# Kernel optimization log

Hardware: AMD Instinct MI355X
Metric: run time of the kernel (lower is better)

Reference implementation:

```python
import jax, jax.numpy as jnp
import numpy as np

H = 1024          # hidden_size
I = 2048          # intermediate_size
E = 8             # num_experts
K = 2             # num_experts_per_token
B, S = 4, 4096


def setup_inputs() -> dict:
    key = jax.random.key(0)
    ks = jax.random.split(key, 5)
    scale = 0.02
    return {
        "hidden_states": jax.random.normal(ks[0], (B, S, H), dtype=jnp.float32),
        "gate_w": jax.random.normal(ks[1], (H, E), dtype=jnp.float32) * scale,      # router gate (Linear, no bias), stored [in,out]
        "gate_proj_w": jax.random.normal(ks[2], (E, H, I), dtype=jnp.float32) * scale,
        "up_proj_w": jax.random.normal(ks[3], (E, H, I), dtype=jnp.float32) * scale,
        "down_proj_w": jax.random.normal(ks[4], (E, I, H), dtype=jnp.float32) * scale,
    }


def reference(hidden_states, gate_w, gate_proj_w, up_proj_w, down_proj_w):
    b, s, h = hidden_states.shape
    x = hidden_states.reshape(-1, h)                      # (T, H), T = b*s
    T = x.shape[0]

    # --- Router: softmax over experts, top-k, renormalize ---
    logits = x @ gate_w                                    # (T, E)
    probs = jax.nn.softmax(logits, axis=-1)
    topk_w, topk_idx = jax.lax.top_k(probs, K)             # (T, K)
    topk_w = topk_w / jnp.sum(topk_w, axis=-1, keepdims=True)

    # Per-token combine weight for each expert (0 if not routed).
    # topk indices are distinct, so scatter-add == scatter-set here.
    combine = jnp.zeros((T, E), dtype=x.dtype).at[
        jnp.arange(T)[:, None], topk_idx
    ].add(topk_w)                                          # (T, E)

    # --- Experts: SwiGLU FFN, weighted combine ---
    out = jnp.zeros_like(x)
    for e in range(E):  # small fixed expert count
        g = jax.nn.silu(x @ gate_proj_w[e])                # (T, I)
        u = x @ up_proj_w[e]                               # (T, I)
        y = (g * u) @ down_proj_w[e]                       # (T, H)
        out = out + y * combine[:, e:e + 1]
    return out.reshape(b, s, h)
```

## Files before the change

### kernel.cpp

```cpp
#include <hip/hip_runtime.h>
#include <hip/hip_bf16.h>

#define T_TOK 16384
#define H_DIM 1024
#define I_DIM 2048
#define E_NUM 8

typedef short short8 __attribute__((ext_vector_type(8)));
typedef float f32x4 __attribute__((ext_vector_type(4)));

__device__ __forceinline__ unsigned short f2bf(float f) {
  union { float f; unsigned u; } v; v.f = f;
  unsigned r = (v.u + 0x7FFFu + ((v.u >> 16) & 1u)) >> 16;
  return (unsigned short)r;
}
__device__ __forceinline__ float bf2f(unsigned short u) {
  union { unsigned u; float f; } v; v.u = ((unsigned)u) << 16;
  return v.f;
}

__device__ __forceinline__ void gload16(const void* g, void* l) {
  __builtin_amdgcn_global_load_lds(
      (const __attribute__((address_space(1))) unsigned int*)g,
      (__attribute__((address_space(3))) unsigned int*)l, 16, 0, 0);
}

#define VMCNT4() asm volatile("s_waitcnt vmcnt(4)" ::: "memory")
#define VMCNT0() asm volatile("s_waitcnt vmcnt(0)" ::: "memory")
#define BAR() __builtin_amdgcn_s_barrier()
#define SCHEDFENCE() __builtin_amdgcn_sched_barrier(0)

__global__ __launch_bounds__(256) void convert_router_kernel(
    const float* __restrict__ x, const float* __restrict__ gw,
    unsigned short* __restrict__ xb,
    int* __restrict__ tke, float* __restrict__ pwv) {
  const int tid = threadIdx.x;
  const int lane = tid & 63;
  const int wv = tid >> 6;
  const int t = blockIdx.x * 4 + wv;
  const float* xr = x + (size_t)t * H_DIM;
  unsigned short* xbr = xb + (size_t)t * H_DIM;

  float acc[8] = {0.f, 0.f, 0.f, 0.f, 0.f, 0.f, 0.f, 0.f};
#pragma unroll
  for (int i = 0; i < 4; ++i) {
    int h0 = i * 256 + lane * 4;
    float4 v = *(const float4*)(xr + h0);
    ushort4 o;
    o.x = f2bf(v.x); o.y = f2bf(v.y); o.z = f2bf(v.z); o.w = f2bf(v.w);
    *(ushort4*)(xbr + h0) = o;
    float vv[4] = {v.x, v.y, v.z, v.w};
#pragma unroll
    for (int j = 0; j < 4; ++j) {
      const float4 g0 = *(const float4*)(gw + (size_t)(h0 + j) * 8);
      const float4 g1 = *(const float4*)(gw + (size_t)(h0 + j) * 8 + 4);
      acc[0] += vv[j] * g0.x; acc[1] += vv[j] * g0.y;
      acc[2] += vv[j] * g0.z; acc[3] += vv[j] * g0.w;
      acc[4] += vv[j] * g1.x; acc[5] += vv[j] * g1.y;
      acc[6] += vv[j] * g1.z; acc[7] += vv[j] * g1.w;
    }
  }
#pragma unroll
  for (int e = 0; e < 8; ++e) {
#pragma unroll
    for (int off = 32; off; off >>= 1) acc[e] += __shfl_xor(acc[e], off);
  }
  int e1 = 0; float l1 = acc[0];
#pragma unroll
  for (int e = 1; e < 8; ++e) if (acc[e] > l1) { l1 = acc[e]; e1 = e; }
  int first_non = (e1 == 0) ? 1 : 0;
  int e2 = first_non; float l2 = acc[first_non];
#pragma unroll
  for (int e = 0; e < 8; ++e) {
    if (e == e1 || e == first_non) continue;
    if (acc[e] > l2) { l2 = acc[e]; e2 = e; }
  }
  float r = expf(l2 - l1);
  float w1 = 1.f / (1.f + r);
  float w2 = r / (1.f + r);
  if (lane == 0) {
    pwv[2 * t] = w1;
    pwv[2 * t + 1] = w2;
    tke[t] = e1 | (e2 << 4);
  }
}

__global__ __launch_bounds__(256) void build_lists_kernel(
    const int* __restrict__ tke, int* __restrict__ list, int* __restrict__ cnt) {
  const int t = blockIdx.x * 256 + threadIdx.x;
  const int lane = threadIdx.x & 63;
  const int pk = tke[t];
  const int ee[2] = {pk & 15, (pk >> 4) & 15};
#pragma unroll
  for (int phase = 0; phase < 2; ++phase) {
    const int e = ee[phase];
    const int pid = 2 * t + phase;
#pragma unroll
    for (int ex = 0; ex < E_NUM; ++ex) {
      unsigned long long mask = __ballot(e == ex);
      if (e == ex) {
        unsigned long long below = mask & ((1ull << lane) - 1ull);
        int rank = __popcll(below);
        int leader = __ffsll((unsigned long long)mask) - 1;
        int base = 0;
        if (lane == leader) base = atomicAdd(&cnt[ex], __popcll(mask));
        base = __shfl(base, leader);
        list[ex * T_TOK + base + rank] = pid;
      }
    }
  }
}

__global__ __launch_bounds__(256) void transpose_convert(
    const float* __restrict__ src, unsigned short* __restrict__ dst, int K, int N) {
  __shared__ float t[128][65];
  const int e = blockIdx.x, kt = blockIdx.y, nt = blockIdx.z;
  const float* s = src + (size_t)e * K * N + (size_t)(kt * 128) * N + nt * 64;
  unsigned short* d = dst + (size_t)e * N * K + (size_t)(nt * 64) * K + kt * 128;
  const int tid = threadIdx.x;
  const int lr = tid & 15, row = tid >> 4;
#pragma unroll
  for (int p = 0; p < 8; ++p) {
    int k = row + p * 16;
    float4 v = *(const float4*)(s + (size_t)k * N + lr * 4);
    t[k][lr * 4 + 0] = v.x;
    t[k][lr * 4 + 1] = v.y;
    t[k][lr * 4 + 2] = v.z;
    t[k][lr * 4 + 3] = v.w;
  }
  __syncthreads();
  const int kc = tid & 15, nr = tid >> 4;
#pragma unroll
  for (int p = 0; p < 4; ++p) {
    int n = nr + p * 16;
    short8 o;
#pragma unroll
    for (int j = 0; j < 8; ++j) o[j] = (short)f2bf(t[kc * 8 + j][n]);
    *(short8*)&d[(size_t)n * K + kc * 8] = o;
  }
}

__global__ __launch_bounds__(256, 3) void gemm_gateup(
    const unsigned short* __restrict__ xb, const unsigned short* __restrict__ wgt,
    const unsigned short* __restrict__ wut, const int* __restrict__ list,
    const int* __restrict__ cnt, const float* __restrict__ pwv,
    unsigned short* __restrict__ hbuf) {
  __shared__ unsigned short As[2][128 * 32];
  __shared__ unsigned short Bg[2][64 * 32];
  __shared__ unsigned short Bu[2][64 * 32];
  __shared__ int rows_s[128];
  __shared__ float pws[128];

  const int tid = threadIdx.x;
  const int e = blockIdx.y >> 7;
  const int mt = blockIdx.y & 127;
  const int ce = cnt[e];
  if (mt * 128 >= ce) return;
  const int n0 = blockIdx.x * 64;

  if (tid < 128) {
    int idx = mt * 128 + tid;
    int pid = list[e * T_TOK + (idx < ce ? idx : 0)];
    rows_s[tid] = pid;
    pws[tid] = pwv[pid];
  }
  __syncthreads();

  const int s0 = tid, s1 = 256 + tid;
  const int q0 = (((s0 & 3) ^ ((s0 >> 3) & 3)) * 8);
  const int q1 = (((s1 & 3) ^ ((s1 >> 3) & 3)) * 8);
  const int tok0 = rows_s[s0 >> 2] >> 1, tok1 = rows_s[s1 >> 2] >> 1;

  const unsigned short* wg_base = wgt + ((size_t)e * I_DIM + n0) * H_DIM;
  const unsigned short* wu_base = wut + ((size_t)e * I_DIM + n0) * H_DIM;
  const unsigned short* a_src0 = xb + (size_t)tok0 * H_DIM + q0;
  const unsigned short* a_src1 = xb + (size_t)tok1 * H_DIM + q1;
  const unsigned short* g_src0 = wg_base + (size_t)(s0 >> 2) * H_DIM + q0;
  const unsigned short* u_src0 = wu_base + (size_t)(s0 >> 2) * H_DIM + q0;

#define STAGE_GU(b, k0)                         \
  do {                                          \
    gload16(a_src0 + (k0), &As[b][s0 * 8]);     \
    gload16(a_src1 + (k0), &As[b][s1 * 8]);     \
    gload16(g_src0 + (k0), &Bg[b][s0 * 8]);     \
    gload16(u_src0 + (k0), &Bu[b][s0 * 8]);     \
  } while (0)

  f32x4 zero = {0.f, 0.f, 0.f, 0.f};
  f32x4 accg[4][2], accu[4][2];
#pragma unroll
  for (int m = 0; m < 4; ++m)
#pragma unroll
    for (int n = 0; n < 2; ++n) { accg[m][n] = zero; accu[m][n] = zero; }

  const int lane = tid & 63;
  const int wv = tid >> 6;
  const int wr = (wv >> 1) * 64;
  const int wc = (wv & 1) * 32;
  const int lr = lane & 15;
  const int lks = (((lane >> 4) ^ ((lr >> 1) & 3)) * 8);

  STAGE_GU(0, 0);

  for (int kt = 0; kt < H_DIM / 32; ++kt) {
    const int cur = kt & 1;
    if (kt < H_DIM / 32 - 1) {
      STAGE_GU(cur ^ 1, (kt + 1) * 32);
      VMCNT4();
    } else {
      VMCNT0();
    }
    BAR();
    SCHEDFENCE();
    const unsigned short* Ab = As[cur];
    const unsigned short* Bgb = Bg[cur];
    const unsigned short* Bub = Bu[cur];
    short8 a[4], bg[2], bu[2];
#pragma unroll
    for (int m = 0; m < 4; ++m)
      a[m] = *(const short8*)&Ab[(wr + m * 16 + lr) * 32 + lks];
#pragma unroll
    for (int n = 0; n < 2; ++n) {
      bg[n] = *(const short8*)&Bgb[(wc + n * 16 + lr) * 32 + lks];
      bu[n] = *(const short8*)&Bub[(wc + n * 16 + lr) * 32 + lks];
    }
    __builtin_amdgcn_s_setprio(1);
#pragma unroll
    for (int m = 0; m < 4; ++m)
#pragma unroll
      for (int n = 0; n < 2; ++n) {
        accg[m][n] = __builtin_amdgcn_mfma_f32_16x16x32_bf16(a[m], bg[n], accg[m][n], 0, 0, 0);
        accu[m][n] = __builtin_amdgcn_mfma_f32_16x16x32_bf16(a[m], bu[n], accu[m][n], 0, 0, 0);
      }
    __builtin_amdgcn_s_setprio(0);
    BAR();
  }
#undef STAGE_GU

  const int rr = (lane >> 4) * 4;
#pragma unroll
  for (int m = 0; m < 4; ++m) {
#pragma unroll
    for (int j = 0; j < 4; ++j) {
      int tr = wr + m * 16 + rr + j;
      if (mt * 128 + tr < ce) {
        int pid = rows_s[tr];
        float wgt_r = pws[tr];
        size_t rowb = (size_t)pid * I_DIM + n0 + wc;
#pragma unroll
        for (int n = 0; n < 2; ++n) {
          float g = accg[m][n][j];
          float u = accu[m][n][j];
          float hv = wgt_r * (g / (1.f + __expf(-g))) * u;
          hbuf[rowb + n * 16 + lr] = f2bf(hv);
        }
      }
    }
  }
}

__global__ __launch_bounds__(256, 3) void gemm_down(
    const unsigned short* __restrict__ hbuf, const unsigned short* __restrict__ wdt,
    const int* __restrict__ list, const int* __restrict__ cnt,
    unsigned short* __restrict__ pbuf) {
  __shared__ unsigned short As[2][128 * 32];
  __shared__ unsigned short Bs[2][128 * 32];
  __shared__ int rows_s[128];

  const int tid = threadIdx.x;
  const int e = blockIdx.y >> 7;
  const int mt = blockIdx.y & 127;
  const int ce = cnt[e];
  if (mt * 128 >= ce) return;
  const int n0 = blockIdx.x * 128;

  if (tid < 128) {
    int idx = mt * 128 + tid;
    rows_s[tid] = list[e * T_TOK + (idx < ce ? idx : 0)];
  }
  __syncthreads();

  const int s0 = tid, s1 = 256 + tid;
  const int r0s = s0 >> 2, r1s = s1 >> 2;
  const int q0 = (((s0 & 3) ^ ((s0 >> 3) & 3)) * 8);
  const int q1 = (((s1 & 3) ^ ((s1 >> 3) & 3)) * 8);
  const int pid0 = rows_s[r0s], pid1 = rows_s[r1s];

  const unsigned short* wd_base = wdt + ((size_t)e * H_DIM + n0) * I_DIM;
  const unsigned short* a_src0 = hbuf + (size_t)pid0 * I_DIM + q0;
  const unsigned short* a_src1 = hbuf + (size_t)pid1 * I_DIM + q1;
  const unsigned short* b_src0 = wd_base + (size_t)r0s * I_DIM + q0;
  const unsigned short* b_src1 = wd_base + (size_t)r1s * I_DIM + q1;

#define STAGE_DN(b, k0)                         \
  do {                                          \
    gload16(a_src0 + (k0), &As[b][s0 * 8]);     \
    gload16(a_src1 + (k0), &As[b][s1 * 8]);     \
    gload16(b_src0 + (k0), &Bs[b][s0 * 8]);     \
    gload16(b_src1 + (k0), &Bs[b][s1 * 8]);     \
  } while (0)

  f32x4 zero = {0.f, 0.f, 0.f, 0.f};
  f32x4 acc[4][4];
#pragma unroll
  for (int m = 0; m < 4; ++m)
#pragma unroll
    for (int n = 0; n < 4; ++n) acc[m][n] = zero;

  const int lane = tid & 63;
  const int wv = tid >> 6;
  const int wr = (wv >> 1) * 64;
  const int wc = (wv & 1) * 64;
  const int lr = lane & 15;
  const int lks = (((lane >> 4) ^ ((lr >> 1) & 3)) * 8);

  STAGE_DN(0, 0);

  for (int kt = 0; kt < I_DIM / 32; ++kt) {
    const int cur = kt & 1;
    if (kt < I_DIM / 32 - 1) {
      STAGE_DN(cur ^ 1, (kt + 1) * 32);
      VMCNT4();
    } else {
      VMCNT0();
    }
    BAR();
    SCHEDFENCE();
    const unsigned short* Ab = As[cur];
    const unsigned short* Bb = Bs[cur];
    short8 a[4], b[4];
#pragma unroll
    for (int m = 0; m < 4; ++m)
      a[m] = *(const short8*)&Ab[(wr + m * 16 + lr) * 32 + lks];
#pragma unroll
    for (int n = 0; n < 4; ++n)
      b[n] = *(const short8*)&Bb[(wc + n * 16 + lr) * 32 + lks];
    __builtin_amdgcn_s_setprio(1);
#pragma unroll
    for (int m = 0; m < 4; ++m)
#pragma unroll
      for (int n = 0; n < 4; ++n)
        acc[m][n] = __builtin_amdgcn_mfma_f32_16x16x32_bf16(a[m], b[n], acc[m][n], 0, 0, 0);
    __builtin_amdgcn_s_setprio(0);
    BAR();
  }
#undef STAGE_DN

  const int rr = (lane >> 4) * 4;
#pragma unroll
  for (int m = 0; m < 4; ++m) {
#pragma unroll
    for (int j = 0; j < 4; ++j) {
      int tr = wr + m * 16 + rr + j;
      if (mt * 128 + tr < ce) {
        int pid = rows_s[tr];
        unsigned short* orow = pbuf + (size_t)pid * H_DIM + n0 + wc;
#pragma unroll
        for (int n = 0; n < 4; ++n)
          orow[n * 16 + lr] = f2bf(acc[m][n][j]);
      }
    }
  }
}

__global__ __launch_bounds__(256) void combine_kernel(float* __restrict__ out) {
  const int tid = threadIdx.x, lane = tid & 63, wv = tid >> 6;
  const int t = blockIdx.x * 4 + wv;
  const unsigned short* p = (const unsigned short*)out;
  const unsigned short* r0 = p + (size_t)(2 * t) * H_DIM + lane * 16;
  const unsigned short* r1 = p + (size_t)(2 * t + 1) * H_DIM + lane * 16;
  short8 a0 = *(const short8*)r0;
  short8 a1 = *(const short8*)(r0 + 8);
  short8 b0 = *(const short8*)r1;
  short8 b1 = *(const short8*)(r1 + 8);
  float res[16];
#pragma unroll
  for (int j = 0; j < 8; ++j) {
    res[j] = bf2f((unsigned short)a0[j]) + bf2f((unsigned short)b0[j]);
    res[8 + j] = bf2f((unsigned short)a1[j]) + bf2f((unsigned short)b1[j]);
  }
  float* orow = out + (size_t)t * H_DIM + lane * 16;
#pragma unroll
  for (int j = 0; j < 4; ++j) {
    float4 w = {res[4 * j], res[4 * j + 1], res[4 * j + 2], res[4 * j + 3]};
    ((float4*)orow)[j] = w;
  }
}

extern "C" void kernel_launch(void* const* d_in, const int* in_sizes, int n_in,
                              void* d_out, int out_size, void* d_ws, size_t ws_size,
                              hipStream_t stream) {
  const float* x = (const float*)d_in[0];
  const float* gw = (const float*)d_in[1];
  const float* wgf = (const float*)d_in[2];
  const float* wuf = (const float*)d_in[3];
  const float* wdf = (const float*)d_in[4];

  const size_t off_xb   = 0;
  const size_t off_wdt  = 33554432;
  const size_t off_h    = 67108864;
  const size_t off_list = 201326592;
  const size_t off_pw   = 201850880;
  const size_t off_cnt  = 201981952;
  const size_t ws_needed = off_cnt + 64;
  if (ws_size < ws_needed) return;

  char* ws = (char*)d_ws;
  unsigned short* xb   = (unsigned short*)(ws + off_xb);
  unsigned short* wdt  = (unsigned short*)(ws + off_wdt);
  unsigned short* hbuf = (unsigned short*)(ws + off_h);
  int*   list = (int*)(ws + off_list);
  float* pwv  = (float*)(ws + off_pw);
  int*   cnt  = (int*)(ws + off_cnt);
  int*   tke  = (int*)(ws + off_h);

  unsigned short* wgt = (unsigned short*)d_out;
  unsigned short* wut = (unsigned short*)d_out + (size_t)E_NUM * H_DIM * I_DIM;
  unsigned short* pbuf = (unsigned short*)d_out;

  hipMemsetAsync(cnt, 0, E_NUM * sizeof(int), stream);

  convert_router_kernel<<<T_TOK / 4, 256, 0, stream>>>(x, gw, xb, tke, pwv);
  build_lists_kernel<<<T_TOK / 256, 256, 0, stream>>>(tke, list, cnt);
  transpose_convert<<<dim3(E_NUM, H_DIM / 128, I_DIM / 64), 256, 0, stream>>>(
      wgf, wgt, H_DIM, I_DIM);
  transpose_convert<<<dim3(E_NUM, H_DIM / 128, I_DIM / 64), 256, 0, stream>>>(
      wuf, wut, H_DIM, I_DIM);
  transpose_convert<<<dim3(E_NUM, I_DIM / 128, H_DIM / 64), 256, 0, stream>>>(
      wdf, wdt, I_DIM, H_DIM);

  gemm_gateup<<<dim3(I_DIM / 64, E_NUM * 128), 256, 0, stream>>>(
      xb, wgt, wut, list, cnt, pwv, hbuf);

  gemm_down<<<dim3(H_DIM / 128, E_NUM * 128), 256, 0, stream>>>(
      hbuf, wdt, list, cnt, pbuf);

  combine_kernel<<<T_TOK / 4, 256, 0, stream>>>((float*)d_out);
}
```

Before: 749.6 us.

## Rewrite down-projection GEMM as 256x256 tile with 8 waves and staged LDS reads

The down-projection kernel moves from 128x128 tiles with 4 waves and K-step 32 to 256x256 tiles with 8 waves (512 threads) and K-step 64, using an XOR-swizzled LDS layout. Fragment loads from LDS are split into four phases interleaved with MFMA groups and barriers, in the style of an 8-wave ping-pong schedule. The goal is more data reuse per global load and better overlap of LDS reads with matrix math. In exchange the kernel uses much more LDS (128KB double-buffered), launches fewer blocks, and pads more rows per expert, which can hurt occupancy and wave quantization.

Result: no change. 760.2 us (+1.4%).

```diff
diff --git a/kernel.cpp b/kernel.cpp
--- a/kernel.cpp
+++ b/kernel.cpp
@@ -27,8 +27,11 @@
 
 #define VMCNT4() asm volatile("s_waitcnt vmcnt(4)" ::: "memory")
 #define VMCNT0() asm volatile("s_waitcnt vmcnt(0)" ::: "memory")
+#define LGKM0()  asm volatile("s_waitcnt lgkmcnt(0)" ::: "memory")
 #define BAR() __builtin_amdgcn_s_barrier()
 #define SCHEDFENCE() __builtin_amdgcn_sched_barrier(0)
+#define PRIO1() __builtin_amdgcn_s_setprio(1)
+#define PRIO0() __builtin_amdgcn_s_setprio(0)
 
 __global__ __launch_bounds__(256) void convert_router_kernel(
     const float* __restrict__ x, const float* __restrict__ gw,
@@ -224,7 +227,7 @@
       bg[n] = *(const short8*)&Bgb[(wc + n * 16 + lr) * 32 + lks];
       bu[n] = *(const short8*)&Bub[(wc + n * 16 + lr) * 32 + lks];
     }
-    __builtin_amdgcn_s_setprio(1);
+    PRIO1();
 #pragma unroll
     for (int m = 0; m < 4; ++m)
 #pragma unroll
@@ -232,7 +235,7 @@
         accg[m][n] = __builtin_amdgcn_mfma_f32_16x16x32_bf16(a[m], bg[n], accg[m][n], 0, 0, 0);
         accu[m][n] = __builtin_amdgcn_mfma_f32_16x16x32_bf16(a[m], bu[n], accu[m][n], 0, 0, 0);
       }
-    __builtin_amdgcn_s_setprio(0);
+    PRIO0();
     BAR();
   }
 #undef STAGE_GU
@@ -259,102 +262,161 @@
   }
 }
 
-__global__ __launch_bounds__(256, 3) void gemm_down(
+__global__ __launch_bounds__(512, 2) void gemm_down8(
     const unsigned short* __restrict__ hbuf, const unsigned short* __restrict__ wdt,
     const int* __restrict__ list, const int* __restrict__ cnt,
     unsigned short* __restrict__ pbuf) {
-  __shared__ unsigned short As[2][128 * 32];
-  __shared__ unsigned short Bs[2][128 * 32];
-  __shared__ int rows_s[128];
+  __shared__ unsigned short As[2][256 * 64];
+  __shared__ unsigned short Bs[2][256 * 64];
+  __shared__ int rows_s[256];
 
   const int tid = threadIdx.x;
-  const int e = blockIdx.y >> 7;
-  const int mt = blockIdx.y & 127;
+  const int e = blockIdx.y >> 6;
+  const int mt = blockIdx.y & 63;
   const int ce = cnt[e];
-  if (mt * 128 >= ce) return;
-  const int n0 = blockIdx.x * 128;
-
-  if (tid < 128) {
-    int idx = mt * 128 + tid;
+  if (mt * 256 >= ce) return;
+  const int n0 = blockIdx.x * 256;
+
+  if (tid < 256) {
+    int idx = mt * 256 + tid;
     rows_s[tid] = list[e * T_TOK + (idx < ce ? idx : 0)];
   }
   __syncthreads();
 
-  const int s0 = tid, s1 = 256 + tid;
-  const int r0s = s0 >> 2, r1s = s1 >> 2;
-  const int q0 = (((s0 & 3) ^ ((s0 >> 3) & 3)) * 8);
-  const int q1 = (((s1 & 3) ^ ((s1 >> 3) & 3)) * 8);
-  const int pid0 = rows_s[r0s], pid1 = rows_s[r1s];
-
   const unsigned short* wd_base = wdt + ((size_t)e * H_DIM + n0) * I_DIM;
-  const unsigned short* a_src0 = hbuf + (size_t)pid0 * I_DIM + q0;
-  const unsigned short* a_src1 = hbuf + (size_t)pid1 * I_DIM + q1;
-  const unsigned short* b_src0 = wd_base + (size_t)r0s * I_DIM + q0;
-  const unsigned short* b_src1 = wd_base + (size_t)r1s * I_DIM + q1;
-
-#define STAGE_DN(b, k0)                         \
-  do {                                          \
-    gload16(a_src0 + (k0), &As[b][s0 * 8]);     \
-    gload16(a_src1 + (k0), &As[b][s1 * 8]);     \
-    gload16(b_src0 + (k0), &Bs[b][s0 * 8]);     \
-    gload16(b_src1 + (k0), &Bs[b][s1 * 8]);     \
+  const unsigned short* a_base[4];
+  const unsigned short* b_base[4];
+#pragma unroll
+  for (int j = 0; j < 4; ++j) {
+    int slot = j * 512 + tid;
+    int row = slot >> 3;
+    int cs = ((slot & 7) ^ (row & 7)) * 8;
+    a_base[j] = hbuf + (size_t)rows_s[row] * I_DIM + cs;
+    b_base[j] = wd_base + (size_t)row * I_DIM + cs;
+  }
+
+#define STAGE8(b, t)                                          \
+  do {                                                        \
+    const int k0_ = (t) * 64;                                 \
+    gload16(a_base[0] + k0_, &As[b][(0 * 512 + tid) * 8]);    \
+    gload16(a_base[1] + k0_, &As[b][(1 * 512 + tid) * 8]);    \
+    gload16(a_base[2] + k0_, &As[b][(2 * 512 + tid) * 8]);    \
+    gload16(a_base[3] + k0_, &As[b][(3 * 512 + tid) * 8]);    \
+    gload16(b_base[0] + k0_, &Bs[b][(0 * 512 + tid) * 8]);    \
+    gload16(b_base[1] + k0_, &Bs[b][(1 * 512 + tid) * 8]);    \
+    gload16(b_base[2] + k0_, &Bs[b][(2 * 512 + tid) * 8]);    \
+    gload16(b_base[3] + k0_, &Bs[b][(3 * 512 + tid) * 8]);    \
   } while (0)
 
   f32x4 zero = {0.f, 0.f, 0.f, 0.f};
-  f32x4 acc[4][4];
-#pragma unroll
-  for (int m = 0; m < 4; ++m)
+  f32x4 acc[8][4];
+#pragma unroll
+  for (int m = 0; m < 8; ++m)
 #pragma unroll
     for (int n = 0; n < 4; ++n) acc[m][n] = zero;
 
   const int lane = tid & 63;
   const int wv = tid >> 6;
-  const int wr = (wv >> 1) * 64;
-  const int wc = (wv & 1) * 64;
+  const int wm = wv >> 2;
+  const int wn = wv & 3;
   const int lr = lane & 15;
-  const int lks = (((lane >> 4) ^ ((lr >> 1) & 3)) * 8);
-
-  STAGE_DN(0, 0);
-
-  for (int kt = 0; kt < I_DIM / 32; ++kt) {
-    const int cur = kt & 1;
-    if (kt < I_DIM / 32 - 1) {
-      STAGE_DN(cur ^ 1, (kt + 1) * 32);
-      VMCNT4();
-    } else {
-      VMCNT0();
-    }
+  const int lg = lane >> 4;
+  const int pc0 = ((lg) ^ (lr & 7)) * 8;
+  const int pc1 = ((lg + 4) ^ (lr & 7)) * 8;
+
+  short8 a[4][2], b[4][2];
+
+  STAGE8(0, 0);
+
+  const int NT = I_DIM / 64;
+  for (int t = 0; t < NT; ++t) {
+    const int cur = t & 1;
+    VMCNT0();
     BAR();
     SCHEDFENCE();
+    if (t + 1 < NT) STAGE8(cur ^ 1, t + 1);
+
     const unsigned short* Ab = As[cur];
     const unsigned short* Bb = Bs[cur];
-    short8 a[4], b[4];
+
+#pragma unroll
+    for (int m = 0; m < 4; ++m) {
+      int row = (wm * 128 + m * 16 + lr) * 64;
+      a[m][0] = *(const short8*)&Ab[row + pc0];
+      a[m][1] = *(const short8*)&Ab[row + pc1];
+    }
+#pragma unroll
+    for (int n = 0; n < 2; ++n) {
+      int row = (wn * 64 + n * 16 + lr) * 64;
+      b[n][0] = *(const short8*)&Bb[row + pc0];
+      b[n][1] = *(const short8*)&Bb[row + pc1];
+    }
+    BAR(); LGKM0();
+    PRIO1();
 #pragma unroll
     for (int m = 0; m < 4; ++m)
-      a[m] = *(const short8*)&Ab[(wr + m * 16 + lr) * 32 + lks];
-#pragma unroll
-    for (int n = 0; n < 4; ++n)
-      b[n] = *(const short8*)&Bb[(wc + n * 16 + lr) * 32 + lks];
-    __builtin_amdgcn_s_setprio(1);
+#pragma unroll
+      for (int n = 0; n < 2; ++n) {
+        acc[m][n] = __builtin_amdgcn_mfma_f32_16x16x32_bf16(a[m][0], b[n][0], acc[m][n], 0, 0, 0);
+        acc[m][n] = __builtin_amdgcn_mfma_f32_16x16x32_bf16(a[m][1], b[n][1], acc[m][n], 0, 0, 0);
+      }
+    PRIO0();
+
+#pragma unroll
+    for (int n = 2; n < 4; ++n) {
+      int row = (wn * 64 + n * 16 + lr) * 64;
+      b[n][0] = *(const short8*)&Bb[row + pc0];
+      b[n][1] = *(const short8*)&Bb[row + pc1];
+    }
+    BAR(); LGKM0();
+    PRIO1();
 #pragma unroll
     for (int m = 0; m < 4; ++m)
 #pragma unroll
-      for (int n = 0; n < 4; ++n)
-        acc[m][n] = __builtin_amdgcn_mfma_f32_16x16x32_bf16(a[m], b[n], acc[m][n], 0, 0, 0);
-    __builtin_amdgcn_s_setprio(0);
-    BAR();
-  }
-#undef STAGE_DN
-
-  const int rr = (lane >> 4) * 4;
-#pragma unroll
-  for (int m = 0; m < 4; ++m) {
+      for (int n = 2; n < 4; ++n) {
+        acc[m][n] = __builtin_amdgcn_mfma_f32_16x16x32_bf16(a[m][0], b[n][0], acc[m][n], 0, 0, 0);
+        acc[m][n] = __builtin_amdgcn_mfma_f32_16x16x32_bf16(a[m][1], b[n][1], acc[m][n], 0, 0, 0);
+      }
+    PRIO0();
+
+#pragma unroll
+    for (int m = 0; m < 4; ++m) {
+      int row = (wm * 128 + (m + 4) * 16 + lr) * 64;
+      a[m][0] = *(const short8*)&Ab[row + pc0];
+      a[m][1] = *(const short8*)&Ab[row + pc1];
+    }
+    BAR(); LGKM0();
+    PRIO1();
+#pragma unroll
+    for (int m = 0; m < 4; ++m)
+#pragma unroll
+      for (int n = 0; n < 2; ++n) {
+        acc[m + 4][n] = __builtin_amdgcn_mfma_f32_16x16x32_bf16(a[m][0], b[n][0], acc[m + 4][n], 0, 0, 0);
+        acc[m + 4][n] = __builtin_amdgcn_mfma_f32_16x16x32_bf16(a[m][1], b[n][1], acc[m + 4][n], 0, 0, 0);
+      }
+    PRIO0();
+
+    PRIO1();
+#pragma unroll
+    for (int m = 0; m < 4; ++m)
+#pragma unroll
+      for (int n = 2; n < 4; ++n) {
+        acc[m + 4][n] = __builtin_amdgcn_mfma_f32_16x16x32_bf16(a[m][0], b[n][0], acc[m + 4][n], 0, 0, 0);
+        acc[m + 4][n] = __builtin_amdgcn_mfma_f32_16x16x32_bf16(a[m][1], b[n][1], acc[m + 4][n], 0, 0, 0);
+      }
+    PRIO0();
+  }
+#undef STAGE8
+
+  const int rr = lg * 4;
+#pragma unroll
+  for (int m = 0; m < 8; ++m) {
 #pragma unroll
     for (int j = 0; j < 4; ++j) {
-      int tr = wr + m * 16 + rr + j;
-      if (mt * 128 + tr < ce) {
+      int tr = wm * 128 + m * 16 + rr + j;
+      if (mt * 256 + tr < ce) {
         int pid = rows_s[tr];
-        unsigned short* orow = pbuf + (size_t)pid * H_DIM + n0 + wc;
+        unsigned short* orow = pbuf + (size_t)pid * H_DIM + n0 + wn * 64;
 #pragma unroll
         for (int n = 0; n < 4; ++n)
           orow[n * 16 + lr] = f2bf(acc[m][n][j]);
@@ -432,7 +494,7 @@
   gemm_gateup<<<dim3(I_DIM / 64, E_NUM * 128), 256, 0, stream>>>(
       xb, wgt, wut, list, cnt, pwv, hbuf);
 
-  gemm_down<<<dim3(H_DIM / 128, E_NUM * 128), 256, 0, stream>>>(
+  gemm_down8<<<dim3(H_DIM / 256, E_NUM * 64), 512, 0, stream>>>(
       hbuf, wdt, list, cnt, pbuf);
 
   combine_kernel<<<T_TOK / 4, 256, 0, stream>>>((float*)d_out);
```
